# Kernel optimization log

Measured on AMD Instinct MI355X. Metric: run time of the kernel, lower is better.

The kernel has to match this reference:

```python
import jax, jax.numpy as jnp
import numpy as np

B = 1024          # number of graphs
N = 64            # atoms per graph
NUM_NODES = B * N
HID = 256         # hidden_channels
H1 = HID // 2
E = 2_097_152     # edges (avg degree 32)


def _xavier(k, fan_in, fan_out):
    lim = np.sqrt(6.0 / (fan_in + fan_out)).astype(np.float32)
    return jax.random.uniform(k, (fan_in, fan_out), jnp.float32, -lim, lim)


def setup_inputs() -> dict:
    key = jax.random.key(0)
    ks = jax.random.split(key, 6)
    node_features = jax.random.normal(ks[0], (NUM_NODES, HID), jnp.float32)
    edge_index = jax.random.randint(ks[1], (2, E), 0, NUM_NODES)
    batch = jnp.repeat(jnp.arange(B), N)  # sorted graph ids, equal-size graphs
    W1 = _xavier(ks[2], HID + 1, H1); b1 = jnp.zeros((H1,), jnp.float32)
    W2 = _xavier(ks[3], H1, H1);      b2 = jnp.zeros((H1,), jnp.float32)
    W3 = _xavier(ks[4], H1, 1);       b3 = jnp.zeros((1,), jnp.float32)
    kT = jnp.ones((1,), jnp.float32)
    return {"node_features": node_features, "W1": W1, "b1": b1, "W2": W2,
            "b2": b2, "W3": W3, "b3": b3, "kT": kT,
            "edge_index": edge_index, "batch": batch}


def reference(node_features, W1, b1, W2, b2, W3, b3, kT, edge_index, batch):
    num_nodes = node_features.shape[0]
    # node degree: count of occurrences as source node
    deg = jnp.zeros((num_nodes,), jnp.float32).at[edge_index[0]].add(1.0)
    # per-graph atom counts and segment start offsets (n_atoms_i)
    counts = jax.ops.segment_sum(jnp.ones((num_nodes,), jnp.float32), batch,
                                 num_segments=B)
    start = jnp.cumsum(counts) - counts  # exclusive cumsum
    # stable per-graph sort of degrees in one shot: lexsort keys, primary=batch
    order = jnp.lexsort((deg, batch))  # global original indices, sorted by (batch, deg)
    # connectivity feature: local original index of the k-th smallest-degree
    # node in its graph, normalized by graph size (matches sorted_index / n_atoms_i)
    conn = (order.astype(jnp.float32) - start[batch]) / counts[batch]
    # MLP(hidden+1 -> hid/2 -> hid/2 -> 1) with silu
    x = jnp.concatenate([conn[:, None], node_features], axis=-1)  # [nodes, HID+1]
    h = jax.nn.silu(x @ W1 + b1)
    h = jax.nn.silu(h @ W2 + b2)
    logits = (h @ W3 + b3)[:, 0] / kT[0]
    # per-graph (segment) softmax
    m = jax.ops.segment_max(logits, batch, num_segments=B)
    e = jnp.exp(logits - m[batch])
    s = jax.ops.segment_sum(e, batch, num_segments=B)
    return e / s[batch]  # concat of per-graph softmaxed probabilities
```

## Files before the change

kernel.cpp:

```cpp
#include <hip/hip_runtime.h>

#define NB 1024
#define NPG 64
#define NUM_NODES 65536
#define HID 256
#define H1DIM 128
#define NE 2097152
#define GH 256

typedef __attribute__((ext_vector_type(8))) _Float16 f16x8;
typedef __attribute__((ext_vector_type(4))) float f32x4;

#define PART_OFF (128*1024)
#define CONN_OFF (PART_OFF + 16*1024*1024)

__device__ __forceinline__ void dma16(const void* g, void* l) {
    __builtin_amdgcn_global_load_lds(
        (const __attribute__((address_space(1))) unsigned int*)g,
        (__attribute__((address_space(3))) unsigned int*)l, 16, 0, 0);
}

__global__ __launch_bounds__(512) void prep_hist_kernel(
    const float* __restrict__ W1, const float* __restrict__ W2,
    _Float16* __restrict__ wf,
    const int4* __restrict__ src4, unsigned int* __restrict__ partials)
{
    __shared__ unsigned int h[16384];
    const int bx = blockIdx.x;
    const int tid = threadIdx.x;

    if (bx < GH) {
        uint4* h4 = (uint4*)h;
#pragma unroll
        for (int i = 0; i < 8; ++i) h4[tid + i * 512] = make_uint4(0u, 0u, 0u, 0u);
        __syncthreads();
        const int4* p = src4 + bx * ((NE / 4) / GH);
#pragma unroll
        for (int i = 0; i < 4; ++i) {
            int4 v = p[tid + i * 512];
            atomicAdd(&h[v.x >> 2], 1u << ((v.x & 3) * 8));
            atomicAdd(&h[v.y >> 2], 1u << ((v.y & 3) * 8));
            atomicAdd(&h[v.z >> 2], 1u << ((v.z & 3) * 8));
            atomicAdd(&h[v.w >> 2], 1u << ((v.w & 3) * 8));
        }
        __syncthreads();
        uint4* dst = (uint4*)partials;
#pragma unroll
        for (int i = 0; i < 8; ++i) {
            const int j = tid + i * 512;
            const int g = j >> 2, u = j & 3;
            dst[(size_t)g * (GH * 4) + bx * 4 + u] = h4[j];
        }
    } else {
        const int bb = bx - GH;
        const int L = tid & 63;
        const int c = L & 15;
        const int j = tid >> 6;
        const float* srcw;
        _Float16* dstw;
        int kt, nt;
        if (bb < 64) { kt = bb >> 3; nt = bb & 7; srcw = W1 + H1DIM; dstw = wf + bb * 512; }
        else { int bc = bb - 64; kt = bc >> 3; nt = bc & 7; srcw = W2; dstw = wf + 32768 + bc * 512; }
        const int k = kt * 32 + (L >> 4) * 8 + j;
        const int n = nt * 16 + c;
        dstw[L * 8 + j] = (_Float16)srcw[k * H1DIM + n];
    }
}

__global__ __launch_bounds__(256) void degree_rank_kernel(
    const unsigned int* __restrict__ partials, float* __restrict__ conns_g)
{
    __shared__ unsigned int dp[4][16][16];
    __shared__ unsigned int degs[4][NPG];
    const int b = blockIdx.x;
    const int t = threadIdx.x;
    const int wd = t & 15, sg = t >> 4;

#pragma unroll
    for (int gg = 0; gg < 4; ++gg) {
        const unsigned int* pg = partials + (size_t)(b * 4 + gg) * (GH * 16);
        unsigned int s = 0;
#pragma unroll
        for (int i = 0; i < 16; ++i) s += pg[(sg * 16 + i) * 16 + wd];
        dp[gg][sg][wd] = s;
    }
    __syncthreads();
    if (t < 64) {
        const int gp = t >> 4, w2 = t & 15;
        unsigned int s = 0;
#pragma unroll
        for (int k = 0; k < 16; ++k) s += dp[gp][k][w2];
        degs[gp][w2 * 4 + 0] = s & 255u;
        degs[gp][w2 * 4 + 1] = (s >> 8) & 255u;
        degs[gp][w2 * 4 + 2] = (s >> 16) & 255u;
        degs[gp][w2 * 4 + 3] = s >> 24;
    }
    __syncthreads();
    {
        const int gg = t >> 6, i = t & 63;
        unsigned int di = degs[gg][i];
        int rk = 0;
#pragma unroll 8
        for (int j = 0; j < NPG; ++j) {
            unsigned int dj = degs[gg][j];
            rk += (int)((dj < di) | ((dj == di) & (j < i)));
        }
        conns_g[(size_t)(b * 4 + gg) * NPG + rk] = (float)i * (1.0f / 64.0f);
    }
}

__global__ __launch_bounds__(512, 4) void mlp_softmax_kernel(
    const float* __restrict__ feat,
    const float* __restrict__ W1, const float* __restrict__ b1,
    const float* __restrict__ b2,
    const float* __restrict__ W3, const float* __restrict__ b3,
    const float* __restrict__ kT,
    const _Float16* __restrict__ wf,
    const float* __restrict__ conns_g,
    float* __restrict__ out)
{
    __shared__ _Float16 wfs[32768];
    __shared__ float logits_s[2][NPG];

    const int tid = threadIdx.x;
    const int L = tid & 63;
    const int w = __builtin_amdgcn_readfirstlane(tid >> 6);
    const int h = w >> 2;
    const int w4 = w & 3;
    const int q = L >> 4;
    const int c = L & 15;
    const int g0 = blockIdx.x * 2;
    const int node0 = g0 * NPG;

    const float* featw = &feat[(size_t)(node0 + h * 64 + w4 * 16 + c) * HID + q * 8];
    f16x8 af[8];
#pragma unroll
    for (int kt = 0; kt < 8; ++kt) {
        float4 A = *(const float4*)(featw + kt * 32);
        float4 B = *(const float4*)(featw + kt * 32 + 4);
        f16x8 v = { (_Float16)A.x, (_Float16)A.y, (_Float16)A.z, (_Float16)A.w,
                    (_Float16)B.x, (_Float16)B.y, (_Float16)B.z, (_Float16)B.w };
        af[kt] = v;
    }

#pragma unroll
    for (int i = 0; i < 8; ++i)
        dma16(&wf[(i * 512 + tid) * 8], &wfs[(i * 512 + w * 64) * 8]);

    float cn[4];
#pragma unroll
    for (int r = 0; r < 4; ++r)
        cn[r] = conns_g[(size_t)(g0 + h) * NPG + w4 * 16 + q * 4 + r];

    float b1v[8], w1r0[8];
#pragma unroll
    for (int nt = 0; nt < 8; ++nt) {
        b1v[nt]  = b1[nt * 16 + c];
        w1r0[nt] = W1[nt * 16 + c];
    }

    __syncthreads();

    f32x4 acc[8];
#pragma unroll
    for (int nt = 0; nt < 8; ++nt)
#pragma unroll
        for (int r = 0; r < 4; ++r)
            acc[nt][r] = fmaf(cn[r], w1r0[nt], b1v[nt]);

#pragma unroll
    for (int kt = 0; kt < 8; ++kt) {
#pragma unroll
        for (int nt = 0; nt < 8; ++nt) {
            f16x8 bfv = *(const f16x8*)&wfs[(kt * 8 + nt) * 512 + L * 8];
            acc[nt] = __builtin_amdgcn_mfma_f32_16x16x32_f16(af[kt], bfv, acc[nt], 0, 0, 0);
        }
    }

    __syncthreads();

#pragma unroll
    for (int i = 0; i < 4; ++i)
        dma16(&wf[32768 + (i * 512 + tid) * 8], &wfs[(i * 512 + w * 64) * 8]);

#pragma unroll
    for (int nt = 0; nt < 8; ++nt) {
        const int ktp = nt >> 1;
        const int lp = (((nt & 1) << 1) + (c >> 3)) * 16 + q * 4;
        const int j = c & 7;
#pragma unroll
        for (int r = 0; r < 4; ++r) {
            float v = acc[nt][r];
            float hv = v / (1.0f + __expf(-v));
            wfs[16384 + w * 2048 + ktp * 512 + (lp + r) * 8 + j] = (_Float16)hv;
        }
    }
    float b2v[8], w3v[8];
#pragma unroll
    for (int nt = 0; nt < 8; ++nt) {
        b2v[nt] = b2[nt * 16 + c];
        w3v[nt] = W3[nt * 16 + c];
    }
    __syncthreads();

    f32x4 acc2[8];
#pragma unroll
    for (int nt = 0; nt < 8; ++nt)
#pragma unroll
        for (int r = 0; r < 4; ++r) acc2[nt][r] = b2v[nt];
#pragma unroll
    for (int kt = 0; kt < 4; ++kt) {
        f16x8 a = *(const f16x8*)&wfs[16384 + w * 2048 + kt * 512 + L * 8];
#pragma unroll
        for (int nt = 0; nt < 8; ++nt) {
            f16x8 bfv = *(const f16x8*)&wfs[(kt * 8 + nt) * 512 + L * 8];
            acc2[nt] = __builtin_amdgcn_mfma_f32_16x16x32_f16(a, bfv, acc2[nt], 0, 0, 0);
        }
    }

    float lg[4] = {0.0f, 0.0f, 0.0f, 0.0f};
#pragma unroll
    for (int nt = 0; nt < 8; ++nt)
#pragma unroll
        for (int r = 0; r < 4; ++r) {
            float v = acc2[nt][r];
            float hv = v / (1.0f + __expf(-v));
            lg[r] = fmaf(hv, w3v[nt], lg[r]);
        }
#pragma unroll
    for (int d = 1; d < 16; d <<= 1)
#pragma unroll
        for (int r = 0; r < 4; ++r) lg[r] += __shfl_xor(lg[r], d, 64);
    if (c == 0) {
#pragma unroll
        for (int r = 0; r < 4; ++r) logits_s[h][w4 * 16 + q * 4 + r] = lg[r];
    }
    __syncthreads();

    if ((tid & 192) == 0) {
        const int hh = tid >> 8, i = tid & 63;
        float s = (logits_s[hh][i] + b3[0]) / kT[0];
        float m = s;
#pragma unroll
        for (int d = 1; d < 64; d <<= 1) m = fmaxf(m, __shfl_xor(m, d, 64));
        float e = __expf(s - m);
        float su = e;
#pragma unroll
        for (int d = 1; d < 64; d <<= 1) su += __shfl_xor(su, d, 64);
        out[node0 + hh * NPG + i] = e / su;
    }
}

extern "C" void kernel_launch(void* const* d_in, const int* in_sizes, int n_in,
                              void* d_out, int out_size, void* d_ws, size_t ws_size,
                              hipStream_t stream)
{
    const float* feat = (const float*)d_in[0];
    const float* W1   = (const float*)d_in[1];
    const float* b1   = (const float*)d_in[2];
    const float* W2   = (const float*)d_in[3];
    const float* b2   = (const float*)d_in[4];
    const float* W3   = (const float*)d_in[5];
    const float* b3   = (const float*)d_in[6];
    const float* kT   = (const float*)d_in[7];
    const int*   ei   = (const int*)d_in[8];

    float* out = (float*)d_out;
    _Float16* wf = (_Float16*)d_ws;
    unsigned int* partials = (unsigned int*)((char*)d_ws + PART_OFF);
    float* conns_g = (float*)((char*)d_ws + CONN_OFF);

    prep_hist_kernel<<<GH + 96, 512, 0, stream>>>(W1, W2, wf, (const int4*)ei,
                                                  partials);
    degree_rank_kernel<<<NB / 4, 256, 0, stream>>>(partials, conns_g);
    mlp_softmax_kernel<<<NB / 2, 512, 0, stream>>>(feat, W1, b1, b2, W3, b3,
                                                   kT, wf, conns_g, out);
}
```

Measured before the change: 137.7 us.

## Fuse degree ranking into MLP kernel and process four graphs per block

Removes the separate degree_rank kernel: the MLP kernel now reduces the histogram partials, ranks degrees and builds connectivity features in shared memory. Each block handles four graphs, with each wave computing two 16-row tiles so every LDS weight fragment feeds two MFMAs. Feature loads are issued early through inline asm so they overlap the weight DMA and the ranking work. This saves one launch and a global round trip, but it doubles register and LDS use per block (launch bounds drop to 2 blocks per CU) and halves the grid to 256 blocks.

Result: no change. 135.9 us (-1.3%).

```diff
diff --git a/kernel.cpp b/kernel.cpp
--- a/kernel.cpp
+++ b/kernel.cpp
@@ -12,7 +12,6 @@
 typedef __attribute__((ext_vector_type(4))) float f32x4;
 
 #define PART_OFF (128*1024)
-#define CONN_OFF (PART_OFF + 16*1024*1024)
 
 __device__ __forceinline__ void dma16(const void* g, void* l) {
     __builtin_amdgcn_global_load_lds(
@@ -67,37 +66,92 @@
     }
 }
 
-__global__ __launch_bounds__(256) void degree_rank_kernel(
-    const unsigned int* __restrict__ partials, float* __restrict__ conns_g)
+__global__ __launch_bounds__(512, 2) void mlp_softmax_kernel(
+    const float* __restrict__ feat,
+    const float* __restrict__ W1, const float* __restrict__ b1,
+    const float* __restrict__ b2,
+    const float* __restrict__ W3, const float* __restrict__ b3,
+    const float* __restrict__ kT,
+    const _Float16* __restrict__ wf,
+    const unsigned int* __restrict__ partials,
+    float* __restrict__ out)
 {
-    __shared__ unsigned int dp[4][16][16];
+    __shared__ _Float16 wfs[49152];
+    __shared__ unsigned int dpart[4][8][16];
     __shared__ unsigned int degs[4][NPG];
-    const int b = blockIdx.x;
-    const int t = threadIdx.x;
-    const int wd = t & 15, sg = t >> 4;
-
-#pragma unroll
-    for (int gg = 0; gg < 4; ++gg) {
-        const unsigned int* pg = partials + (size_t)(b * 4 + gg) * (GH * 16);
+    __shared__ float conns[4][NPG];
+    __shared__ float logits_s[4][NPG];
+
+    const int tid = threadIdx.x;
+    const int L = tid & 63;
+    const int w = __builtin_amdgcn_readfirstlane(tid >> 6);
+    const int h2 = w >> 1;
+    const int tp = (w & 1) * 2;
+    const int q = L >> 4;
+    const int c = L & 15;
+    const int g0 = blockIdx.x * 4;
+    const int node0 = g0 * NPG;
+
+    const float* f0 = &feat[(size_t)(node0 + h2 * 64 + tp * 16 + c) * HID + q * 8];
+    const float* f1 = f0 + 16 * HID;
+    float4 va[32];
+#define LOADF(arr_i, base, byteoff)                                          \
+    asm volatile("global_load_dwordx4 %0, %1, off offset:" #byteoff          \
+                 : "=v"(va[arr_i]) : "v"(base))
+    LOADF(0, f0, 0);    LOADF(1, f0, 16);
+    LOADF(2, f0, 128);  LOADF(3, f0, 144);
+    LOADF(4, f0, 256);  LOADF(5, f0, 272);
+    LOADF(6, f0, 384);  LOADF(7, f0, 400);
+    LOADF(8, f0, 512);  LOADF(9, f0, 528);
+    LOADF(10, f0, 640); LOADF(11, f0, 656);
+    LOADF(12, f0, 768); LOADF(13, f0, 784);
+    LOADF(14, f0, 896); LOADF(15, f0, 912);
+    LOADF(16, f1, 0);   LOADF(17, f1, 16);
+    LOADF(18, f1, 128); LOADF(19, f1, 144);
+    LOADF(20, f1, 256); LOADF(21, f1, 272);
+    LOADF(22, f1, 384); LOADF(23, f1, 400);
+    LOADF(24, f1, 512); LOADF(25, f1, 528);
+    LOADF(26, f1, 640); LOADF(27, f1, 656);
+    LOADF(28, f1, 768); LOADF(29, f1, 784);
+    LOADF(30, f1, 896); LOADF(31, f1, 912);
+#undef LOADF
+
+#pragma unroll
+    for (int i = 0; i < 8; ++i)
+        dma16(&wf[(i * 512 + tid) * 8], &wfs[(i * 512 + w * 64) * 8]);
+
+    {
+        const int gg = tid >> 7;
+        const int t128 = tid & 127;
+        const int wd = t128 & 15, sgr = t128 >> 4;
+        const unsigned int* pg = partials + (size_t)(g0 + gg) * (GH * 16);
         unsigned int s = 0;
 #pragma unroll
-        for (int i = 0; i < 16; ++i) s += pg[(sg * 16 + i) * 16 + wd];
-        dp[gg][sg][wd] = s;
-    }
-    __syncthreads();
-    if (t < 64) {
-        const int gp = t >> 4, w2 = t & 15;
+        for (int i = 0; i < 32; ++i) s += pg[(sgr * 32 + i) * 16 + wd];
+        dpart[gg][sgr][wd] = s;
+    }
+
+    float b1v[8], w1r0[8];
+#pragma unroll
+    for (int nt = 0; nt < 8; ++nt) {
+        b1v[nt]  = b1[nt * 16 + c];
+        w1r0[nt] = W1[nt * 16 + c];
+    }
+
+    __syncthreads();
+    if (tid < 64) {
+        const int gp = tid >> 4, w2 = tid & 15;
         unsigned int s = 0;
 #pragma unroll
-        for (int k = 0; k < 16; ++k) s += dp[gp][k][w2];
+        for (int k = 0; k < 8; ++k) s += dpart[gp][k][w2];
         degs[gp][w2 * 4 + 0] = s & 255u;
         degs[gp][w2 * 4 + 1] = (s >> 8) & 255u;
         degs[gp][w2 * 4 + 2] = (s >> 16) & 255u;
         degs[gp][w2 * 4 + 3] = s >> 24;
     }
     __syncthreads();
-    {
-        const int gg = t >> 6, i = t & 63;
+    if (tid < 256) {
+        const int gg = tid >> 6, i = tid & 63;
         unsigned int di = degs[gg][i];
         int rk = 0;
 #pragma unroll 8
@@ -105,75 +159,46 @@
             unsigned int dj = degs[gg][j];
             rk += (int)((dj < di) | ((dj == di) & (j < i)));
         }
-        conns_g[(size_t)(b * 4 + gg) * NPG + rk] = (float)i * (1.0f / 64.0f);
-    }
-}
-
-__global__ __launch_bounds__(512, 4) void mlp_softmax_kernel(
-    const float* __restrict__ feat,
-    const float* __restrict__ W1, const float* __restrict__ b1,
-    const float* __restrict__ b2,
-    const float* __restrict__ W3, const float* __restrict__ b3,
-    const float* __restrict__ kT,
-    const _Float16* __restrict__ wf,
-    const float* __restrict__ conns_g,
-    float* __restrict__ out)
-{
-    __shared__ _Float16 wfs[32768];
-    __shared__ float logits_s[2][NPG];
-
-    const int tid = threadIdx.x;
-    const int L = tid & 63;
-    const int w = __builtin_amdgcn_readfirstlane(tid >> 6);
-    const int h = w >> 2;
-    const int w4 = w & 3;
-    const int q = L >> 4;
-    const int c = L & 15;
-    const int g0 = blockIdx.x * 2;
-    const int node0 = g0 * NPG;
-
-    const float* featw = &feat[(size_t)(node0 + h * 64 + w4 * 16 + c) * HID + q * 8];
-    f16x8 af[8];
+        conns[gg][rk] = (float)i * (1.0f / 64.0f);
+    }
+    __syncthreads();
+    __builtin_amdgcn_sched_barrier(0);
+
+    f16x8 af0[8], af1[8];
 #pragma unroll
     for (int kt = 0; kt < 8; ++kt) {
-        float4 A = *(const float4*)(featw + kt * 32);
-        float4 B = *(const float4*)(featw + kt * 32 + 4);
-        f16x8 v = { (_Float16)A.x, (_Float16)A.y, (_Float16)A.z, (_Float16)A.w,
-                    (_Float16)B.x, (_Float16)B.y, (_Float16)B.z, (_Float16)B.w };
-        af[kt] = v;
-    }
-
-#pragma unroll
-    for (int i = 0; i < 8; ++i)
-        dma16(&wf[(i * 512 + tid) * 8], &wfs[(i * 512 + w * 64) * 8]);
-
-    float cn[4];
-#pragma unroll
-    for (int r = 0; r < 4; ++r)
-        cn[r] = conns_g[(size_t)(g0 + h) * NPG + w4 * 16 + q * 4 + r];
-
-    float b1v[8], w1r0[8];
-#pragma unroll
-    for (int nt = 0; nt < 8; ++nt) {
-        b1v[nt]  = b1[nt * 16 + c];
-        w1r0[nt] = W1[nt * 16 + c];
-    }
-
-    __syncthreads();
-
-    f32x4 acc[8];
+        float4 A = va[2 * kt], B = va[2 * kt + 1];
+        f16x8 v0 = { (_Float16)A.x, (_Float16)A.y, (_Float16)A.z, (_Float16)A.w,
+                     (_Float16)B.x, (_Float16)B.y, (_Float16)B.z, (_Float16)B.w };
+        af0[kt] = v0;
+        float4 C = va[16 + 2 * kt], D = va[16 + 2 * kt + 1];
+        f16x8 v1 = { (_Float16)C.x, (_Float16)C.y, (_Float16)C.z, (_Float16)C.w,
+                     (_Float16)D.x, (_Float16)D.y, (_Float16)D.z, (_Float16)D.w };
+        af1[kt] = v1;
+    }
+
+    float cn0[4], cn1[4];
+#pragma unroll
+    for (int r = 0; r < 4; ++r) {
+        cn0[r] = conns[h2][tp * 16 + q * 4 + r];
+        cn1[r] = conns[h2][(tp + 1) * 16 + q * 4 + r];
+    }
+    f32x4 acc0[8], acc1[8];
 #pragma unroll
     for (int nt = 0; nt < 8; ++nt)
 #pragma unroll
-        for (int r = 0; r < 4; ++r)
-            acc[nt][r] = fmaf(cn[r], w1r0[nt], b1v[nt]);
+        for (int r = 0; r < 4; ++r) {
+            acc0[nt][r] = fmaf(cn0[r], w1r0[nt], b1v[nt]);
+            acc1[nt][r] = fmaf(cn1[r], w1r0[nt], b1v[nt]);
+        }
 
 #pragma unroll
     for (int kt = 0; kt < 8; ++kt) {
 #pragma unroll
         for (int nt = 0; nt < 8; ++nt) {
             f16x8 bfv = *(const f16x8*)&wfs[(kt * 8 + nt) * 512 + L * 8];
-            acc[nt] = __builtin_amdgcn_mfma_f32_16x16x32_f16(af[kt], bfv, acc[nt], 0, 0, 0);
+            acc0[nt] = __builtin_amdgcn_mfma_f32_16x16x32_f16(af0[kt], bfv, acc0[nt], 0, 0, 0);
+            acc1[nt] = __builtin_amdgcn_mfma_f32_16x16x32_f16(af1[kt], bfv, acc1[nt], 0, 0, 0);
         }
     }
 
@@ -184,15 +209,18 @@
         dma16(&wf[32768 + (i * 512 + tid) * 8], &wfs[(i * 512 + w * 64) * 8]);
 
 #pragma unroll
-    for (int nt = 0; nt < 8; ++nt) {
-        const int ktp = nt >> 1;
-        const int lp = (((nt & 1) << 1) + (c >> 3)) * 16 + q * 4;
-        const int j = c & 7;
-#pragma unroll
-        for (int r = 0; r < 4; ++r) {
-            float v = acc[nt][r];
-            float hv = v / (1.0f + __expf(-v));
-            wfs[16384 + w * 2048 + ktp * 512 + (lp + r) * 8 + j] = (_Float16)hv;
+    for (int set = 0; set < 2; ++set) {
+#pragma unroll
+        for (int nt = 0; nt < 8; ++nt) {
+            const int ktp = nt >> 1;
+            const int lp = (((nt & 1) << 1) + (c >> 3)) * 16 + q * 4;
+            const int j = c & 7;
+#pragma unroll
+            for (int r = 0; r < 4; ++r) {
+                float v = set ? acc1[nt][r] : acc0[nt][r];
+                float hv = v / (1.0f + __expf(-v));
+                wfs[16384 + w * 4096 + set * 2048 + ktp * 512 + (lp + r) * 8 + j] = (_Float16)hv;
+            }
         }
     }
     float b2v[8], w3v[8];
@@ -203,43 +231,52 @@
     }
     __syncthreads();
 
-    f32x4 acc2[8];
+    f32x4 acc20[8], acc21[8];
 #pragma unroll
     for (int nt = 0; nt < 8; ++nt)
 #pragma unroll
-        for (int r = 0; r < 4; ++r) acc2[nt][r] = b2v[nt];
+        for (int r = 0; r < 4; ++r) { acc20[nt][r] = b2v[nt]; acc21[nt][r] = b2v[nt]; }
 #pragma unroll
     for (int kt = 0; kt < 4; ++kt) {
-        f16x8 a = *(const f16x8*)&wfs[16384 + w * 2048 + kt * 512 + L * 8];
+        f16x8 a0 = *(const f16x8*)&wfs[16384 + w * 4096 + kt * 512 + L * 8];
+        f16x8 a1 = *(const f16x8*)&wfs[16384 + w * 4096 + 2048 + kt * 512 + L * 8];
 #pragma unroll
         for (int nt = 0; nt < 8; ++nt) {
             f16x8 bfv = *(const f16x8*)&wfs[(kt * 8 + nt) * 512 + L * 8];
-            acc2[nt] = __builtin_amdgcn_mfma_f32_16x16x32_f16(a, bfv, acc2[nt], 0, 0, 0);
-        }
-    }
-
-    float lg[4] = {0.0f, 0.0f, 0.0f, 0.0f};
+            acc20[nt] = __builtin_amdgcn_mfma_f32_16x16x32_f16(a0, bfv, acc20[nt], 0, 0, 0);
+            acc21[nt] = __builtin_amdgcn_mfma_f32_16x16x32_f16(a1, bfv, acc21[nt], 0, 0, 0);
+        }
+    }
+
+    float lg0[4] = {0,0,0,0}, lg1[4] = {0,0,0,0};
 #pragma unroll
     for (int nt = 0; nt < 8; ++nt)
 #pragma unroll
         for (int r = 0; r < 4; ++r) {
-            float v = acc2[nt][r];
-            float hv = v / (1.0f + __expf(-v));
-            lg[r] = fmaf(hv, w3v[nt], lg[r]);
+            float v0 = acc20[nt][r];
+            lg0[r] = fmaf(v0 / (1.0f + __expf(-v0)), w3v[nt], lg0[r]);
+            float v1 = acc21[nt][r];
+            lg1[r] = fmaf(v1 / (1.0f + __expf(-v1)), w3v[nt], lg1[r]);
         }
 #pragma unroll
     for (int d = 1; d < 16; d <<= 1)
 #pragma unroll
-        for (int r = 0; r < 4; ++r) lg[r] += __shfl_xor(lg[r], d, 64);
+        for (int r = 0; r < 4; ++r) {
+            lg0[r] += __shfl_xor(lg0[r], d, 64);
+            lg1[r] += __shfl_xor(lg1[r], d, 64);
+        }
     if (c == 0) {
 #pragma unroll
-        for (int r = 0; r < 4; ++r) logits_s[h][w4 * 16 + q * 4 + r] = lg[r];
-    }
-    __syncthreads();
-
-    if ((tid & 192) == 0) {
-        const int hh = tid >> 8, i = tid & 63;
-        float s = (logits_s[hh][i] + b3[0]) / kT[0];
+        for (int r = 0; r < 4; ++r) {
+            logits_s[h2][tp * 16 + q * 4 + r] = lg0[r];
+            logits_s[h2][(tp + 1) * 16 + q * 4 + r] = lg1[r];
+        }
+    }
+    __syncthreads();
+
+    if (tid < 256) {
+        const int gg = tid >> 6, i = tid & 63;
+        float s = (logits_s[gg][i] + b3[0]) / kT[0];
         float m = s;
 #pragma unroll
         for (int d = 1; d < 64; d <<= 1) m = fmaxf(m, __shfl_xor(m, d, 64));
@@ -247,7 +284,7 @@
         float su = e;
 #pragma unroll
         for (int d = 1; d < 64; d <<= 1) su += __shfl_xor(su, d, 64);
-        out[node0 + hh * NPG + i] = e / su;
+        out[node0 + gg * NPG + i] = e / su;
     }
 }
 
@@ -268,11 +305,9 @@
     float* out = (float*)d_out;
     _Float16* wf = (_Float16*)d_ws;
     unsigned int* partials = (unsigned int*)((char*)d_ws + PART_OFF);
-    float* conns_g = (float*)((char*)d_ws + CONN_OFF);
 
     prep_hist_kernel<<<GH + 96, 512, 0, stream>>>(W1, W2, wf, (const int4*)ei,
                                                   partials);
-    degree_rank_kernel<<<NB / 4, 256, 0, stream>>>(partials, conns_g);
-    mlp_softmax_kernel<<<NB / 2, 512, 0, stream>>>(feat, W1, b1, b2, W3, b3,
-                                                   kT, wf, conns_g, out);
+    mlp_softmax_kernel<<<NB / 4, 512, 0, stream>>>(feat, W1, b1, b2, W3, b3,
+                                                   kT, wf, partials, out);
 }
```
